# Kernel optimization log

Hardware: AMD Instinct MI355X
Metric: run time of the kernel (lower is better)

## Reference

```python
import jax, jax.numpy as jnp
import numpy as np

ALPHA = 1.8   # Levy stability index (undefined global in source; chosen heavy-tailed)
BETA = 0.0    # symmetric
SIGMA = 0.5
DEPTH = 25
DIM = 64
HID = 100
BATCH = 262144


def _levy_noise(u_raw, w_raw):
    """Chambers-Mallows-Stuck sampler for symmetric alpha-stable (beta=0).
    u_raw, w_raw ~ U(0,1); returns clipped noise, scale=0.1, clamp [-10,10]."""
    U = jnp.pi * (u_raw - 0.5)                       # U(-pi/2, pi/2)
    W = -jnp.log(jnp.clip(w_raw, 1e-12, 1.0))        # Exp(1)
    inv_a = 1.0 / ALPHA
    X = (jnp.sin(ALPHA * U) / jnp.cos(U) ** inv_a) * \
        (jnp.cos(U - ALPHA * U) / jnp.clip(W, 1e-12, None)) ** ((1.0 - ALPHA) * inv_a)
    return jnp.clip(0.1 * X, -10.0, 10.0)


def setup_inputs() -> dict:
    key = jax.random.key(0)
    ks = jax.random.split(key, 8)
    d, h = DIM, HID
    return {
        "x": jax.random.normal(ks[0], (BATCH, d), dtype=jnp.float32),
        "u_raw": jax.random.uniform(ks[1], (DEPTH, d), dtype=jnp.float32),
        "w_raw": jax.random.uniform(ks[2], (DEPTH, d), dtype=jnp.float32),
        "W_down": jax.random.normal(ks[3], (d, d), dtype=jnp.float32) / np.sqrt(d),
        "b_down": jnp.zeros((d,), jnp.float32),
        "W_drift": jax.random.normal(ks[4], (d, d), dtype=jnp.float32) / np.sqrt(d),
        "b_drift": jnp.zeros((d,), jnp.float32),
        "W1": jax.random.normal(ks[5], (d, h), dtype=jnp.float32) / np.sqrt(d),
        "b1": jnp.zeros((h,), jnp.float32),
        "W2": jax.random.normal(ks[6], (h, 1), dtype=jnp.float32) / np.sqrt(h),
        "b2": jnp.zeros((1,), jnp.float32),
    }


def reference(x, u_raw, w_raw, W_down, b_down, W_drift, b_drift, W1, b1, W2, b2):
    dt = 1.0 / DEPTH
    out = x @ W_down + b_down                                   # [B, d]
    # diffusion logit on the INITIAL state, held fixed through the loop
    logit = jax.nn.relu(out @ W1 + b1) @ W2 + b2                # [B, 1]
    scale = SIGMA * jax.nn.sigmoid(logit) * dt ** (1.0 / ALPHA)  # [B, 1]
    noise = _levy_noise(u_raw, w_raw)                           # [DEPTH, d]

    def step(out, n):
        drift = jax.nn.relu(out @ W_drift + b_drift) + out      # DriftNet: relu(lin)+x
        return out + drift * dt + scale * n, None

    out, _ = jax.lax.scan(step, out, noise)
    drift_out = jax.nn.relu(out @ W_drift + b_drift) + out
    return drift_out, out
```

## Files before the change

### kernel.cpp

```cpp
#include <hip/hip_runtime.h>

#define DEPTH 25
#define DIM   64
#define HID   100

typedef _Float16 f16x4 __attribute__((ext_vector_type(4)));
typedef _Float16 f16x8 __attribute__((ext_vector_type(8)));
typedef __fp16   h2    __attribute__((ext_vector_type(2)));
typedef float    f32x4 __attribute__((ext_vector_type(4)));
typedef float    f32x2 __attribute__((ext_vector_type(2)));

__global__ __launch_bounds__(64) void levy_noise_kernel(
    const float* __restrict__ u_raw, const float* __restrict__ w_raw,
    float* __restrict__ noise)
{
    const int idx = blockIdx.x * 64 + threadIdx.x;
    if (idx >= DEPTH * DIM) return;
    float u = u_raw[idx];
    float w = w_raw[idx];
    float U  = 3.14159265358979323846f * (u - 0.5f);
    float Wv = -logf(fminf(fmaxf(w, 1e-12f), 1.0f));
    float t1 = sinf(1.8f * U) / powf(cosf(U), 0.5555555555555556f);
    float ratio = cosf(0.8f * U) / fmaxf(Wv, 1e-12f);
    float X = t1 * powf(ratio, -0.4444444444444444f);
    noise[idx] = fminf(fmaxf(0.1f * X, -10.0f), 10.0f);
}

union frag_u { h2 p[4]; f16x8 v; };

__global__ __launch_bounds__(256, 4) void sdenet_fused(
    const float* __restrict__ x,      const float* __restrict__ noise_g,
    const float* __restrict__ W_down, const float* __restrict__ b_down,
    const float* __restrict__ W_drift,const float* __restrict__ b_drift,
    const float* __restrict__ W1,     const float* __restrict__ b1,
    const float* __restrict__ W2,     const float* __restrict__ b2,
    float* __restrict__ out, int batch)
{
    __shared__ float    noise_lds[DEPTH * DIM];
    __shared__ float    bias_lds[DIM];
    __shared__ _Float16 wdown[4096];
    __shared__ _Float16 wdrift[4096];
    __shared__ _Float16 w1buf[7168];

    const int tid  = threadIdx.x;
    const int wave = tid >> 6;
    const int lane = tid & 63;
    const int r    = lane & 15;
    const int g    = lane >> 4;
    const int row  = blockIdx.x * 64 + wave * 16 + r;
    const int fbase = lane * 8;
    const float dt = 0.04f;

    {
        const float4* src = (const float4*)noise_g;
        float4* dst = (float4*)noise_lds;
        #pragma unroll
        for (int it = 0; it < 2; ++it) {
            int idx = tid + it * 256;
            if (idx < DEPTH * DIM / 4) dst[idx] = src[idx];
        }
    }
    if (tid < DIM) bias_lds[tid] = dt * b_drift[tid];

    for (int idx2 = tid; idx2 < 2048; idx2 += 256) {
        const int fi    = idx2 >> 8;
        const int lane2 = (idx2 >> 2) & 63;
        const int j     = (idx2 & 3) * 2;
        const int m     = (fi >> 1) * 16 + (lane2 & 15);
        const int k     = (fi & 1) * 32 + ((j & 4) ? 16 : 0)
                        + (lane2 >> 4) * 4 + (j & 3);
        *(h2*)(wdown + idx2 * 2) =
            __builtin_amdgcn_cvt_pkrtz(W_down[k * DIM + m],
                                       W_down[(k + 1) * DIM + m]);
        *(h2*)(wdrift + idx2 * 2) =
            __builtin_amdgcn_cvt_pkrtz(dt * W_drift[k * DIM + m],
                                       dt * W_drift[(k + 1) * DIM + m]);
    }
    for (int idx2 = tid; idx2 < 3584; idx2 += 256) {
        const int fi    = idx2 >> 8;
        const int lane2 = (idx2 >> 2) & 63;
        const int j     = (idx2 & 3) * 2;
        const int n     = (fi >> 1) * 16 + (lane2 & 15);
        const int k     = (fi & 1) * 32 + ((j & 4) ? 16 : 0)
                        + (lane2 >> 4) * 4 + (j & 3);
        const float v0 = (n < HID) ? W1[k * HID + n] : 0.0f;
        const float v1 = (n < HID) ? W1[(k + 1) * HID + n] : 0.0f;
        *(h2*)(w1buf + idx2 * 2) = __builtin_amdgcn_cvt_pkrtz(v0, v1);
    }

    float4 xlo[2], xhi[2];
    #pragma unroll
    for (int kt = 0; kt < 2; ++kt) {
        xlo[kt] = *(const float4*)(x + row * DIM + kt * 32 + g * 4);
        xhi[kt] = *(const float4*)(x + row * DIM + kt * 32 + 16 + g * 4);
    }
    __syncthreads();

    f16x8 bfrag[2];
    #pragma unroll
    for (int kt = 0; kt < 2; ++kt) {
        frag_u u;
        u.p[0] = __builtin_amdgcn_cvt_pkrtz(xlo[kt].x, xlo[kt].y);
        u.p[1] = __builtin_amdgcn_cvt_pkrtz(xlo[kt].z, xlo[kt].w);
        u.p[2] = __builtin_amdgcn_cvt_pkrtz(xhi[kt].x, xhi[kt].y);
        u.p[3] = __builtin_amdgcn_cvt_pkrtz(xhi[kt].z, xhi[kt].w);
        bfrag[kt] = u.v;
    }

    f32x2 out2[4][2];
    #pragma unroll
    for (int Mt = 0; Mt < 4; ++Mt) {
        f32x4 acc = *(const f32x4*)(b_down + Mt * 16 + g * 4);
        #pragma unroll
        for (int kt = 0; kt < 2; ++kt)
            acc = __builtin_amdgcn_mfma_f32_16x16x32_f16(
                *(const f16x8*)(wdown + (Mt * 2 + kt) * 512 + fbase),
                bfrag[kt], acc, 0, 0, 0);
        out2[Mt][0][0] = acc[0]; out2[Mt][0][1] = acc[1];
        out2[Mt][1][0] = acc[2]; out2[Mt][1][1] = acc[3];
    }

    auto refresh = [&]() {
        #pragma unroll
        for (int kt = 0; kt < 2; ++kt) {
            frag_u u;
            u.p[0] = __builtin_amdgcn_cvt_pkrtz(out2[2*kt  ][0][0], out2[2*kt  ][0][1]);
            u.p[1] = __builtin_amdgcn_cvt_pkrtz(out2[2*kt  ][1][0], out2[2*kt  ][1][1]);
            u.p[2] = __builtin_amdgcn_cvt_pkrtz(out2[2*kt+1][0][0], out2[2*kt+1][0][1]);
            u.p[3] = __builtin_amdgcn_cvt_pkrtz(out2[2*kt+1][1][0], out2[2*kt+1][1][1]);
            bfrag[kt] = u.v;
        }
    };
    refresh();

    float partial = 0.0f;
    #pragma unroll
    for (int Mt = 0; Mt < 7; ++Mt) {
        f32x4 acc;
        #pragma unroll
        for (int reg = 0; reg < 4; ++reg) {
            const int n = Mt * 16 + g * 4 + reg;
            acc[reg] = (n < HID) ? b1[n] : 0.0f;
        }
        #pragma unroll
        for (int kt = 0; kt < 2; ++kt)
            acc = __builtin_amdgcn_mfma_f32_16x16x32_f16(
                *(const f16x8*)(w1buf + (Mt * 2 + kt) * 512 + fbase),
                bfrag[kt], acc, 0, 0, 0);
        #pragma unroll
        for (int reg = 0; reg < 4; ++reg) {
            const int n = Mt * 16 + g * 4 + reg;
            if (n < HID) partial += fmaxf(acc[reg], 0.0f) * W2[n];
        }
    }
    partial += __shfl_xor(partial, 16);
    partial += __shfl_xor(partial, 32);
    const float logit = partial + b2[0];
    const float scale = 0.5f * (1.0f / (1.0f + expf(-logit)))
                      * powf(0.04f, 1.0f / 1.8f);
    const f32x2 scale2 = { scale, scale };
    const f32x2 c104   = { 1.04f, 1.04f };
    const f32x2 zero2  = { 0.0f, 0.0f };

    f16x8 aWd[4][2];
    #pragma unroll
    for (int Mt = 0; Mt < 4; ++Mt)
        #pragma unroll
        for (int kt = 0; kt < 2; ++kt)
            aWd[Mt][kt] = *(const f16x8*)(wdrift + (Mt * 2 + kt) * 512 + fbase);

    #pragma unroll
    for (int t = 0; t < DEPTH; ++t) {
        f32x4 nz[4];
        #pragma unroll
        for (int Mt = 0; Mt < 4; ++Mt)
            nz[Mt] = *(const f32x4*)(noise_lds + t * DIM + Mt * 16 + g * 4);

        f32x4 acc[4];
        #pragma unroll
        for (int Mt = 0; Mt < 4; ++Mt) {
            acc[Mt] = *(const f32x4*)(bias_lds + Mt * 16 + g * 4);
            acc[Mt] = __builtin_amdgcn_mfma_f32_16x16x32_f16(
                aWd[Mt][0], bfrag[0], acc[Mt], 0, 0, 0);
            acc[Mt] = __builtin_amdgcn_mfma_f32_16x16x32_f16(
                aWd[Mt][1], bfrag[1], acc[Mt], 0, 0, 0);
        }
        #pragma unroll
        for (int Mt = 0; Mt < 4; ++Mt) {
            #pragma unroll
            for (int h = 0; h < 2; ++h) {
                f32x2 a2 = { acc[Mt][2*h], acc[Mt][2*h+1] };
                f32x2 n2 = { nz[Mt][2*h],  nz[Mt][2*h+1] };
                f32x2 rel = __builtin_elementwise_max(a2, zero2);
                f32x2 tmp = __builtin_elementwise_fma(out2[Mt][h], c104, rel);
                out2[Mt][h] = __builtin_elementwise_fma(scale2, n2, tmp);
            }
        }
        refresh();
    }

    const long long out2_off = (long long)batch * DIM;
    #pragma unroll
    for (int Mt = 0; Mt < 4; ++Mt) {
        f32x4 acc = *(const f32x4*)(bias_lds + Mt * 16 + g * 4);
        acc = __builtin_amdgcn_mfma_f32_16x16x32_f16(
            aWd[Mt][0], bfrag[0], acc, 0, 0, 0);
        acc = __builtin_amdgcn_mfma_f32_16x16x32_f16(
            aWd[Mt][1], bfrag[1], acc, 0, 0, 0);
        float o0 = out2[Mt][0][0], o1 = out2[Mt][0][1];
        float o2 = out2[Mt][1][0], o3 = out2[Mt][1][1];
        float4 dv, ov;
        dv.x = fmaf(fmaxf(acc[0], 0.0f), 25.0f, o0);
        dv.y = fmaf(fmaxf(acc[1], 0.0f), 25.0f, o1);
        dv.z = fmaf(fmaxf(acc[2], 0.0f), 25.0f, o2);
        dv.w = fmaf(fmaxf(acc[3], 0.0f), 25.0f, o3);
        ov.x = o0; ov.y = o1; ov.z = o2; ov.w = o3;
        *(float4*)(out + (long long)row * DIM + Mt * 16 + g * 4) = dv;
        *(float4*)(out + out2_off + (long long)row * DIM + Mt * 16 + g * 4) = ov;
    }
}

extern "C" void kernel_launch(void* const* d_in, const int* in_sizes, int n_in,
                              void* d_out, int out_size, void* d_ws, size_t ws_size,
                              hipStream_t stream) {
    const float* x       = (const float*)d_in[0];
    const float* u_raw   = (const float*)d_in[1];
    const float* w_raw   = (const float*)d_in[2];
    const float* W_down  = (const float*)d_in[3];
    const float* b_down  = (const float*)d_in[4];
    const float* W_drift = (const float*)d_in[5];
    const float* b_drift = (const float*)d_in[6];
    const float* W1      = (const float*)d_in[7];
    const float* b1      = (const float*)d_in[8];
    const float* W2      = (const float*)d_in[9];
    const float* b2      = (const float*)d_in[10];
    float* out   = (float*)d_out;
    float* noise = (float*)d_ws;

    const int batch = in_sizes[0] / DIM;
    const int blocks = batch / 64;

    levy_noise_kernel<<<DEPTH, 64, 0, stream>>>(u_raw, w_raw, noise);
    sdenet_fused<<<blocks, 256, 0, stream>>>(
        x, noise, W_down, b_down, W_drift, b_drift,
        W1, b1, W2, b2, out, batch);
}
```

Before: 269.5 us.

## Pre-convert weights to fp16 MFMA fragment layout in a prep kernel

After: 245.7 us. 8.8% less time.

```diff
diff --git a/kernel.cpp b/kernel.cpp
--- a/kernel.cpp
+++ b/kernel.cpp
@@ -26,9 +26,203 @@
     noise[idx] = fminf(fmaxf(0.1f * X, -10.0f), 10.0f);
 }
 
+__global__ __launch_bounds__(256) void preconv_kernel(
+    const float* __restrict__ W_down, const float* __restrict__ W_drift,
+    const float* __restrict__ W1,     const float* __restrict__ b1,
+    const float* __restrict__ W2,
+    _Float16* __restrict__ wpre, float* __restrict__ b1p, float* __restrict__ w2p)
+{
+    const int idx = blockIdx.x * 256 + threadIdx.x;
+    if (idx < 7680) {
+        int rel, kind;
+        if (idx < 2048)      { kind = 0; rel = idx; }
+        else if (idx < 4096) { kind = 1; rel = idx - 2048; }
+        else                 { kind = 2; rel = idx - 4096; }
+        const int fi    = rel >> 8;
+        const int lane2 = (rel >> 2) & 63;
+        const int j     = (rel & 3) * 2;
+        const int m     = (fi >> 1) * 16 + (lane2 & 15);
+        const int k     = (fi & 1) * 32 + ((j & 4) ? 16 : 0)
+                        + (lane2 >> 4) * 4 + (j & 3);
+        float v0, v1;
+        if (kind == 0) {
+            v0 = W_down[k * DIM + m];           v1 = W_down[(k + 1) * DIM + m];
+        } else if (kind == 1) {
+            v0 = 0.04f * W_drift[k * DIM + m];  v1 = 0.04f * W_drift[(k + 1) * DIM + m];
+        } else {
+            v0 = (m < HID) ? W1[k * HID + m] : 0.0f;
+            v1 = (m < HID) ? W1[(k + 1) * HID + m] : 0.0f;
+        }
+        *(h2*)(wpre + idx * 2) = __builtin_amdgcn_cvt_pkrtz(v0, v1);
+    } else if (idx < 7792) {
+        const int i = idx - 7680;
+        b1p[i] = (i < HID) ? b1[i] : 0.0f;
+    } else if (idx < 7904) {
+        const int i = idx - 7792;
+        w2p[i] = (i < HID) ? W2[i] : 0.0f;
+    }
+}
+
 union frag_u { h2 p[4]; f16x8 v; };
 
-__global__ __launch_bounds__(256, 4) void sdenet_fused(
+__global__ __launch_bounds__(256, 4) void sdenet_fused_pre(
+    const float* __restrict__ x,      const float* __restrict__ noise_g,
+    const _Float16* __restrict__ wpre,
+    const float* __restrict__ b_down, const float* __restrict__ b_drift,
+    const float* __restrict__ b1p,    const float* __restrict__ w2p,
+    const float* __restrict__ b2,
+    float* __restrict__ out, int batch)
+{
+    __shared__ float noise_lds[DEPTH * DIM];
+
+    const int tid  = threadIdx.x;
+    const int wave = tid >> 6;
+    const int lane = tid & 63;
+    const int r    = lane & 15;
+    const int g    = lane >> 4;
+    const int row  = blockIdx.x * 64 + wave * 16 + r;
+    const int fbase = lane * 8;
+    const float dt = 0.04f;
+
+    {
+        const float4* src = (const float4*)noise_g;
+        float4* dst = (float4*)noise_lds;
+        dst[tid] = src[tid];
+        if (tid < 144) dst[tid + 256] = src[tid + 256];
+    }
+    float4 xlo[2], xhi[2];
+    #pragma unroll
+    for (int kt = 0; kt < 2; ++kt) {
+        xlo[kt] = *(const float4*)(x + row * DIM + kt * 32 + g * 4);
+        xhi[kt] = *(const float4*)(x + row * DIM + kt * 32 + 16 + g * 4);
+    }
+    __syncthreads();
+
+    f16x8 bfrag[2];
+    #pragma unroll
+    for (int kt = 0; kt < 2; ++kt) {
+        frag_u u;
+        u.p[0] = __builtin_amdgcn_cvt_pkrtz(xlo[kt].x, xlo[kt].y);
+        u.p[1] = __builtin_amdgcn_cvt_pkrtz(xlo[kt].z, xlo[kt].w);
+        u.p[2] = __builtin_amdgcn_cvt_pkrtz(xhi[kt].x, xhi[kt].y);
+        u.p[3] = __builtin_amdgcn_cvt_pkrtz(xhi[kt].z, xhi[kt].w);
+        bfrag[kt] = u.v;
+    }
+
+    f32x2 out2[4][2];
+    #pragma unroll
+    for (int Mt = 0; Mt < 4; ++Mt) {
+        f32x4 acc = *(const f32x4*)(b_down + Mt * 16 + g * 4);
+        #pragma unroll
+        for (int kt = 0; kt < 2; ++kt)
+            acc = __builtin_amdgcn_mfma_f32_16x16x32_f16(
+                *(const f16x8*)(wpre + (Mt * 2 + kt) * 512 + fbase),
+                bfrag[kt], acc, 0, 0, 0);
+        out2[Mt][0][0] = acc[0]; out2[Mt][0][1] = acc[1];
+        out2[Mt][1][0] = acc[2]; out2[Mt][1][1] = acc[3];
+    }
+
+    auto refresh = [&]() {
+        #pragma unroll
+        for (int kt = 0; kt < 2; ++kt) {
+            frag_u u;
+            u.p[0] = __builtin_amdgcn_cvt_pkrtz(out2[2*kt  ][0][0], out2[2*kt  ][0][1]);
+            u.p[1] = __builtin_amdgcn_cvt_pkrtz(out2[2*kt  ][1][0], out2[2*kt  ][1][1]);
+            u.p[2] = __builtin_amdgcn_cvt_pkrtz(out2[2*kt+1][0][0], out2[2*kt+1][0][1]);
+            u.p[3] = __builtin_amdgcn_cvt_pkrtz(out2[2*kt+1][1][0], out2[2*kt+1][1][1]);
+            bfrag[kt] = u.v;
+        }
+    };
+    refresh();
+
+    const _Float16* w1pre = wpre + 8192;
+    float partial = 0.0f;
+    #pragma unroll
+    for (int Mt = 0; Mt < 7; ++Mt) {
+        f32x4 acc = *(const f32x4*)(b1p + Mt * 16 + g * 4);
+        #pragma unroll
+        for (int kt = 0; kt < 2; ++kt)
+            acc = __builtin_amdgcn_mfma_f32_16x16x32_f16(
+                *(const f16x8*)(w1pre + (Mt * 2 + kt) * 512 + fbase),
+                bfrag[kt], acc, 0, 0, 0);
+        #pragma unroll
+        for (int reg = 0; reg < 4; ++reg)
+            partial += fmaxf(acc[reg], 0.0f) * w2p[Mt * 16 + g * 4 + reg];
+    }
+    partial += __shfl_xor(partial, 16);
+    partial += __shfl_xor(partial, 32);
+    const float logit = partial + b2[0];
+    const float scale = 0.5f * (1.0f / (1.0f + expf(-logit)))
+                      * powf(0.04f, 1.0f / 1.8f);
+    const f32x2 scale2 = { scale, scale };
+    const f32x2 c104   = { 1.04f, 1.04f };
+    const f32x2 zero2  = { 0.0f, 0.0f };
+
+    f16x8 aWd[4][2];
+    #pragma unroll
+    for (int Mt = 0; Mt < 4; ++Mt)
+        #pragma unroll
+        for (int kt = 0; kt < 2; ++kt)
+            aWd[Mt][kt] = *(const f16x8*)(wpre + 4096 + (Mt * 2 + kt) * 512 + fbase);
+
+    f32x4 biasd[4];
+    #pragma unroll
+    for (int Mt = 0; Mt < 4; ++Mt) {
+        f32x4 b = *(const f32x4*)(b_drift + Mt * 16 + g * 4);
+        biasd[Mt][0] = b[0] * dt; biasd[Mt][1] = b[1] * dt;
+        biasd[Mt][2] = b[2] * dt; biasd[Mt][3] = b[3] * dt;
+    }
+
+    #pragma unroll
+    for (int t = 0; t < DEPTH; ++t) {
+        f32x4 nz[4];
+        #pragma unroll
+        for (int Mt = 0; Mt < 4; ++Mt)
+            nz[Mt] = *(const f32x4*)(noise_lds + t * DIM + Mt * 16 + g * 4);
+
+        f32x4 acc[4];
+        #pragma unroll
+        for (int Mt = 0; Mt < 4; ++Mt) {
+            acc[Mt] = __builtin_amdgcn_mfma_f32_16x16x32_f16(
+                aWd[Mt][0], bfrag[0], biasd[Mt], 0, 0, 0);
+            acc[Mt] = __builtin_amdgcn_mfma_f32_16x16x32_f16(
+                aWd[Mt][1], bfrag[1], acc[Mt], 0, 0, 0);
+        }
+        #pragma unroll
+        for (int Mt = 0; Mt < 4; ++Mt) {
+            #pragma unroll
+            for (int h = 0; h < 2; ++h) {
+                f32x2 a2 = { acc[Mt][2*h], acc[Mt][2*h+1] };
+                f32x2 n2 = { nz[Mt][2*h],  nz[Mt][2*h+1] };
+                f32x2 rel = __builtin_elementwise_max(a2, zero2);
+                f32x2 tmp = __builtin_elementwise_fma(out2[Mt][h], c104, rel);
+                out2[Mt][h] = __builtin_elementwise_fma(scale2, n2, tmp);
+            }
+        }
+        refresh();
+    }
+
+    const long long out2_off = (long long)batch * DIM;
+    #pragma unroll
+    for (int Mt = 0; Mt < 4; ++Mt) {
+        f32x4 acc = __builtin_amdgcn_mfma_f32_16x16x32_f16(
+            aWd[Mt][0], bfrag[0], biasd[Mt], 0, 0, 0);
+        acc = __builtin_amdgcn_mfma_f32_16x16x32_f16(
+            aWd[Mt][1], bfrag[1], acc, 0, 0, 0);
+        float o0 = out2[Mt][0][0], o1 = out2[Mt][0][1];
+        float o2 = out2[Mt][1][0], o3 = out2[Mt][1][1];
+        float4 dv, ov;
+        dv.x = fmaf(fmaxf(acc[0], 0.0f), 25.0f, o0);
+        dv.y = fmaf(fmaxf(acc[1], 0.0f), 25.0f, o1);
+        dv.z = fmaf(fmaxf(acc[2], 0.0f), 25.0f, o2);
+        dv.w = fmaf(fmaxf(acc[3], 0.0f), 25.0f, o3);
+        ov.x = o0; ov.y = o1; ov.z = o2; ov.w = o3;
+        *(float4*)(out + (long long)row * DIM + Mt * 16 + g * 4) = dv;
+        *(float4*)(out + out2_off + (long long)row * DIM + Mt * 16 + g * 4) = ov;
+    }
+}
+
+__global__ __launch_bounds__(256, 4) void sdenet_fused_fb(
     const float* __restrict__ x,      const float* __restrict__ noise_g,
     const float* __restrict__ W_down, const float* __restrict__ b_down,
     const float* __restrict__ W_drift,const float* __restrict__ b_drift,
@@ -235,13 +429,25 @@
     const float* W2      = (const float*)d_in[9];
     const float* b2      = (const float*)d_in[10];
     float* out   = (float*)d_out;
-    float* noise = (float*)d_ws;
+
+    float*     noise = (float*)d_ws;
+    _Float16*  wpre  = (_Float16*)((char*)d_ws + 6400);
+    float*     b1p   = (float*)((char*)d_ws + 37120);
+    float*     w2p   = (float*)((char*)d_ws + 37568);
 
     const int batch = in_sizes[0] / DIM;
     const int blocks = batch / 64;
 
     levy_noise_kernel<<<DEPTH, 64, 0, stream>>>(u_raw, w_raw, noise);
-    sdenet_fused<<<blocks, 256, 0, stream>>>(
-        x, noise, W_down, b_down, W_drift, b_drift,
-        W1, b1, W2, b2, out, batch);
+
+    if (ws_size >= 38016) {
+        preconv_kernel<<<31, 256, 0, stream>>>(W_down, W_drift, W1, b1, W2,
+                                               wpre, b1p, w2p);
+        sdenet_fused_pre<<<blocks, 256, 0, stream>>>(
+            x, noise, wpre, b_down, b_drift, b1p, w2p, b2, out, batch);
+    } else {
+        sdenet_fused_fb<<<blocks, 256, 0, stream>>>(
+            x, noise, W_down, b_down, W_drift, b_drift,
+            W1, b1, W2, b2, out, batch);
+    }
 }
```
